# Kernel optimization log

Measured on AMD Instinct MI355X. Metric: run time of the kernel, lower is better.

The kernel has to match this reference:

```python
import jax, jax.numpy as jnp
import numpy as np

B, A, H = 128, 24, 256
N, E = B * A, B * A * A
MAX_ATOMS, TIME_DIM, TEXT_DIM, NFREQ, NLAYERS = 103, 256, 128, 10, 4
DIS_DIM = NFREQ * 2 * 3  # 60
EDGE_IN = 2 * H + 9 + DIS_DIM  # 581


def setup_inputs() -> dict:
    key = jax.random.key(0)
    ks = iter(jax.random.split(key, 40))
    def nrm(shape, fan_in):
        return jax.random.normal(next(ks), shape, jnp.float32) / np.sqrt(fan_in).astype(np.float32)
    # fully-connected block-diagonal edges per graph (incl. self-loops), as dense_to_sparse(block_diag(ones))
    ii = jnp.repeat(jnp.arange(A, dtype=jnp.int32), A)
    jj = jnp.tile(jnp.arange(A, dtype=jnp.int32), A)
    off = (jnp.arange(B, dtype=jnp.int32) * A)[:, None]
    edges = jnp.stack([(off + ii[None, :]).reshape(-1), (off + jj[None, :]).reshape(-1)])  # [2,E]
    node2graph = jnp.repeat(jnp.arange(B, dtype=jnp.int32), A)  # [N]
    edge2graph = node2graph[edges[0]]  # [E]
    return dict(
        atom_types=jax.random.normal(next(ks), (N, MAX_ATOMS), jnp.float32),
        frac_coords=jax.random.uniform(next(ks), (N, 3), jnp.float32),
        lattices=jax.random.normal(next(ks), (B, 3, 3), jnp.float32),
        t=jax.random.normal(next(ks), (B, TIME_DIM), jnp.float32),
        text_embeds=jax.random.normal(next(ks), (B, TEXT_DIM), jnp.float32),
        w_emb=nrm((H, MAX_ATOMS), MAX_ATOMS), b_emb=jnp.zeros((H,), jnp.float32),
        w_cond=nrm((2 * H, TIME_DIM + TEXT_DIM), TIME_DIM + TEXT_DIM), b_cond=jnp.zeros((2 * H,), jnp.float32),
        w_proj=nrm((H, H), H), b_proj=jnp.zeros((H,), jnp.float32),
        film_g=jnp.ones((H,), jnp.float32), film_b=jnp.zeros((H,), jnp.float32),
        edge_w1=nrm((NLAYERS, H, EDGE_IN), EDGE_IN), edge_b1=jnp.zeros((NLAYERS, H), jnp.float32),
        edge_w2=nrm((NLAYERS, H, H), H), edge_b2=jnp.zeros((NLAYERS, H), jnp.float32),
        node_w1=nrm((NLAYERS, H, 2 * H), 2 * H), node_b1=jnp.zeros((NLAYERS, H), jnp.float32),
        node_w2=nrm((NLAYERS, H, H), H), node_b2=jnp.zeros((NLAYERS, H), jnp.float32),
        w_coord=nrm((3, H), H), w_latt=nrm((9, H), H),
        w_type=nrm((MAX_ATOMS, H), H), b_type=jnp.zeros((MAX_ATOMS,), jnp.float32),
        edges=edges, node2graph=node2graph, edge2graph=edge2graph,
    )


def _layernorm(x, g, b):
    mu = jnp.mean(x, -1, keepdims=True)
    v = jnp.mean((x - mu) ** 2, -1, keepdims=True)
    return (x - mu) * jax.lax.rsqrt(v + 1e-5) * g + b


def reference(atom_types, frac_coords, lattices, t, text_embeds,
              w_emb, b_emb, w_cond, b_cond, w_proj, b_proj, film_g, film_b,
              edge_w1, edge_b1, edge_w2, edge_b2, node_w1, node_b1, node_w2, node_b2,
              w_coord, w_latt, w_type, b_type, edges, node2graph, edge2graph):
    silu = jax.nn.silu
    e0, e1 = edges[0], edges[1]
    # gen_edges (fc): periodic fractional difference per edge
    frac_diff = (frac_coords[e1] - frac_coords[e0]) % 1.0  # [E,3]
    # SinusoidsEmbedding (detached in the original)
    freqs = 2.0 * jnp.pi * jnp.arange(NFREQ, dtype=jnp.float32)
    emb = (frac_diff[..., None] * freqs).reshape(frac_diff.shape[0], 3 * NFREQ)
    demb = jax.lax.stop_gradient(jnp.concatenate([jnp.sin(emb), jnp.cos(emb)], -1))  # [E,60]
    # lattice inner products (ip=True), gathered per edge
    lat_ips = jnp.einsum('bij,bkj->bik', lattices, lattices).reshape(-1, 9)
    lat_e = lat_ips[edge2graph]  # [E,9]
    # FiLM conditioning (identical every layer) -- repeat_interleave per atom == gather by node2graph
    cond = silu(jnp.concatenate([t, text_embeds], -1) @ w_cond.T + b_cond)[node2graph]  # [N,2H]
    scale, shift = cond[:, :H], cond[:, H:]
    deg = jnp.maximum(jax.ops.segment_sum(jnp.ones((e0.shape[0],), jnp.float32), e0, num_segments=N), 1.0)
    nf = atom_types @ w_emb.T + b_emb  # smooth node embedding: Linear(max_atoms, H)
    for i in range(NLAYERS):
        # FiLM layer
        y = _layernorm(nf @ w_proj.T + b_proj, film_g, film_b)
        nf = nf + silu(y * scale + shift)
        # CSPLayer edge model: gather -> concat -> 2-layer MLP
        ein = jnp.concatenate([nf[e0], nf[e1], lat_e, demb], -1)  # [E, 581]
        ef = silu(ein @ edge_w1[i].T + edge_b1[i])
        ef = silu(ef @ edge_w2[i].T + edge_b2[i])
        # node model: scatter_mean over source nodes, then 2-layer MLP, residual
        agg = jax.ops.segment_sum(ef, e0, num_segments=N) / deg[:, None]
        no = silu(jnp.concatenate([nf, agg], -1) @ node_w1[i].T + node_b1[i])
        no = silu(no @ node_w2[i].T + node_b2[i])
        nf = nf + no
    coords_out = nf @ w_coord.T  # [N,3]
    gfeat = jax.ops.segment_sum(nf, node2graph, num_segments=B) / jnp.float32(A)  # scatter mean over graphs
    lattice_out = (gfeat @ w_latt.T).reshape(-1, 3, 3)
    lattice_out = jnp.einsum('bij,bjk->bik', lattice_out, lattices)  # ip=True
    atom_types_out = nf @ w_type.T + b_type  # [N,103]
    return atom_types_out, lattice_out, coords_out, nf
```

## Files before the change

### kernel.cpp

```cpp
#include <hip/hip_runtime.h>
#include <math.h>

#define B_      128
#define A_      24
#define N_      3072
#define NLAYERS 4

#define OFF_COND    0
#define OFF_LATW    65536
#define OFF_NFMIDH  196608
#define OFF_AGGH    589824
#define OFF_PARTIH  983040
#define OFF_PARTJH  1376256
#define OFF_W1LATT  1769472
#define OFF_PW1A    1778688
#define OFF_PW1B    1909760
#define OFF_PW1D    2040832
#define OFF_PW2     2073600
#define OFF_PWPROJ  2204672
#define OFF_PNW1    2237440
#define OFF_PNW2    2499584
#define OFF_PWEMB   2630656
#define OFF_PWCOND  2647040
#define OFF_PWTYPE  2745344

#define OUT_TYPES  0
#define OUT_LATT   316416
#define OUT_COORD  317568
#define OUT_NF     326784

typedef __attribute__((ext_vector_type(8))) short bf16x8;
typedef __attribute__((ext_vector_type(4))) float f32x4;

__device__ __forceinline__ float silu_f(float x) { return x / (1.0f + __expf(-x)); }
__device__ __forceinline__ unsigned short f2bf(float x) {
    unsigned int u = __float_as_uint(x);
    return (unsigned short)((u + 0x7FFFu + ((u >> 16) & 1u)) >> 16);
}
__device__ __forceinline__ float bf2f(unsigned short h) {
    return __uint_as_float(((unsigned int)h) << 16);
}

__global__ void k_prep(const float* w_emb, const float* w_cond, const float* w_proj,
                       const float* ew1, const float* ew2, const float* nw1, const float* nw2,
                       const float* w_type, float* ws) {
    int idx = blockIdx.x * blockDim.x + threadIdx.x;
    unsigned short* pu = (unsigned short*)ws;
    int i = idx;
    if (i < 9216)   { int l = i / 2304, r = (i % 2304) / 256, h = i % 256;
                      ws[OFF_W1LATT + i] = ew1[((size_t)l * 256 + h) * 581 + 512 + r]; return; }        i -= 9216;
    if (i < 262144) { int l = i >> 16, r = i & 65535, ks = r >> 13, r2 = r & 8191,
                      nt = r2 >> 9, r3 = r2 & 511, lane = r3 >> 3, j = r3 & 7;
                      int k = ks * 32 + (lane >> 4) * 8 + j, n = nt * 16 + (lane & 15);
                      pu[(size_t)OFF_PW1A * 2 + i] = f2bf(ew1[((size_t)l * 256 + n) * 581 + k]); return; } i -= 262144;
    if (i < 262144) { int l = i >> 16, r = i & 65535, ks = r >> 13, r2 = r & 8191,
                      nt = r2 >> 9, r3 = r2 & 511, lane = r3 >> 3, j = r3 & 7;
                      int k = ks * 32 + (lane >> 4) * 8 + j, n = nt * 16 + (lane & 15);
                      pu[(size_t)OFF_PW1B * 2 + i] = f2bf(ew1[((size_t)l * 256 + n) * 581 + 256 + k]); return; } i -= 262144;
    if (i < 65536)  { int l = i >> 14, r = i & 16383, ks = r >> 13, r2 = r & 8191,
                      nt = r2 >> 9, r3 = r2 & 511, lane = r3 >> 3, j = r3 & 7;
                      int kp = ks * 32 + (lane >> 4) * 8 + j, n = nt * 16 + (lane & 15);
                      float v = (kp < 60) ? ew1[((size_t)l * 256 + n) * 581 + 521 + kp] : 0.0f;
                      pu[(size_t)OFF_PW1D * 2 + i] = f2bf(v); return; }                                  i -= 65536;
    if (i < 262144) { int l = i >> 16, r = i & 65535, ks = r >> 13, r2 = r & 8191,
                      nt = r2 >> 9, r3 = r2 & 511, lane = r3 >> 3, j = r3 & 7;
                      int k = ks * 32 + (lane >> 4) * 8 + j, n = nt * 16 + (lane & 15);
                      pu[(size_t)OFF_PW2 * 2 + i] = f2bf(ew2[((size_t)l * 256 + n) * 256 + k]); return; } i -= 262144;
    if (i < 65536)  { int ks = i >> 13, r2 = i & 8191,
                      nt = r2 >> 9, r3 = r2 & 511, lane = r3 >> 3, j = r3 & 7;
                      int k = ks * 32 + (lane >> 4) * 8 + j, n = nt * 16 + (lane & 15);
                      pu[(size_t)OFF_PWPROJ * 2 + i] = f2bf(w_proj[(size_t)n * 256 + k]); return; }      i -= 65536;
    if (i < 524288) { int l = i >> 17, r = i & 131071, ks = r >> 13, r2 = r & 8191,
                      nt = r2 >> 9, r3 = r2 & 511, lane = r3 >> 3, j = r3 & 7;
                      int k = ks * 32 + (lane >> 4) * 8 + j, n = nt * 16 + (lane & 15);
                      pu[(size_t)OFF_PNW1 * 2 + i] = f2bf(nw1[((size_t)l * 256 + n) * 512 + k]); return; } i -= 524288;
    if (i < 262144) { int l = i >> 16, r = i & 65535, ks = r >> 13, r2 = r & 8191,
                      nt = r2 >> 9, r3 = r2 & 511, lane = r3 >> 3, j = r3 & 7;
                      int k = ks * 32 + (lane >> 4) * 8 + j, n = nt * 16 + (lane & 15);
                      pu[(size_t)OFF_PNW2 * 2 + i] = f2bf(nw2[((size_t)l * 256 + n) * 256 + k]); return; } i -= 262144;
    if (i < 32768)  { int ks = i >> 13, r2 = i & 8191,
                      nt = r2 >> 9, r3 = r2 & 511, lane = r3 >> 3, j = r3 & 7;
                      int k = ks * 32 + (lane >> 4) * 8 + j, n = nt * 16 + (lane & 15);
                      float v = (k < 103) ? w_emb[(size_t)n * 103 + k] : 0.0f;
                      pu[(size_t)OFF_PWEMB * 2 + i] = f2bf(v); return; }                                 i -= 32768;
    if (i < 196608) { int ks = i / 16384, r2 = i & 16383,
                      nt = r2 >> 9, r3 = r2 & 511, lane = r3 >> 3, j = r3 & 7;
                      int k = ks * 32 + (lane >> 4) * 8 + j, n = nt * 16 + (lane & 15);
                      pu[(size_t)OFF_PWCOND * 2 + i] = f2bf(w_cond[(size_t)n * 384 + k]); return; }      i -= 196608;
    { int ks = i / 3584, r2 = i % 3584,
      nt = r2 >> 9, r3 = r2 & 511, lane = r3 >> 3, j = r3 & 7;
      int k = ks * 32 + (lane >> 4) * 8 + j, a = nt * 16 + (lane & 15);
      float v = (a < 103) ? w_type[(size_t)a * 256 + k] : 0.0f;
      pu[(size_t)OFF_PWTYPE * 2 + i] = f2bf(v); }
}

__global__ void __launch_bounds__(256) k_setup(const float* lat, const float* t_in, const float* tx,
                                               const float* b_cond, float* ws) {
    __shared__ __align__(16) unsigned short s_ct[16][392];
    __shared__ float s_lat[16][9];
    int tid = threadIdx.x, w = tid >> 6, ln = tid & 63;
    int l15 = ln & 15, g = ln >> 4;
    int g0 = blockIdx.x * 16;
    if (tid < 144) {
        int gl = tid / 9, r = tid % 9, ii = r / 3, kk = r % 3;
        const float* L = lat + (g0 + gl) * 9;
        s_lat[gl][r] = L[ii*3+0]*L[kk*3+0] + L[ii*3+1]*L[kk*3+1] + L[ii*3+2]*L[kk*3+2];
    }
    for (int idx = tid; idx < 16 * 384; idx += 256) {
        int row = idx / 384, k = idx % 384;
        float v = (k < 256) ? t_in[(size_t)(g0 + row) * 256 + k] : tx[(size_t)(g0 + row) * 128 + (k - 256)];
        s_ct[row][k] = f2bf(v);
    }
    __syncthreads();
    for (int idx = tid; idx < 16384; idx += 256) {
        int l = idx >> 12, gl = (idx >> 8) & 15, h = idx & 255;
        float a = 0.f;
#pragma unroll
        for (int r = 0; r < 9; r++) a += s_lat[gl][r] * ws[OFF_W1LATT + (l * 9 + r) * 256 + h];
        ws[OFF_LATW + (size_t)(l * 128 + g0 + gl) * 256 + h] = a;
    }
    const unsigned short* pc = (const unsigned short*)ws + (size_t)OFF_PWCOND * 2;
    f32x4 acc[8] = {};
    for (int ks = 0; ks < 12; ks++) {
        bf16x8 a = *(const bf16x8*)&s_ct[l15][ks * 32 + g * 8];
#pragma unroll
        for (int q = 0; q < 8; q++) {
            int nt = w * 8 + q;
            bf16x8 bf = *(const bf16x8*)&pc[((size_t)(ks * 32 + nt) * 64 + ln) * 8];
            acc[q] = __builtin_amdgcn_mfma_f32_16x16x32_bf16(a, bf, acc[q], 0, 0, 0);
        }
    }
#pragma unroll
    for (int q = 0; q < 8; q++) {
        int col = w * 128 + q * 16 + l15;
        float bc = b_cond[col];
#pragma unroll
        for (int r = 0; r < 4; r++) {
            int gg = g0 + 4 * g + r;
            ws[OFF_COND + (size_t)gg * 512 + col] = silu_f(acc[q][r] + bc);
        }
    }
}

__global__ void __launch_bounds__(256) k_fnf(int l, const float* at, const float* b_emb,
                                             const float* nb1, const float* nb2,
                                             const float* b_proj, const float* film_g, const float* film_b,
                                             const float* eb1, float* ws) {
    __shared__ __align__(16) unsigned short s_in[16][536];
    __shared__ __align__(16) unsigned short s_h[16][264];
    __shared__ __align__(16) unsigned short s_a[16][264];
    __shared__ float s_nf[16][260];
    __shared__ float s_mu[16], s_rs[16];
    float (*s_c)[268] = (float(*)[268])&s_in[0][0];
    int tid = threadIdx.x, w = tid >> 6, ln = tid & 63;
    int l15 = ln & 15, g = ln >> 4;
    int n0 = blockIdx.x * 16;
    const unsigned short* wsu = (const unsigned short*)ws;
    unsigned short* wsw = (unsigned short*)ws;

    f32x4 accn[4] = {};
    if (l == 0) {
        for (int idx = tid; idx < 16 * 128; idx += 256) {
            int row = idx >> 7, k = idx & 127;
            s_in[row][k] = (k < 103) ? f2bf(at[(size_t)(n0 + row) * 103 + k]) : (unsigned short)0;
        }
        __syncthreads();
        const unsigned short* pe = wsu + (size_t)OFF_PWEMB * 2;
        for (int ks = 0; ks < 4; ks++) {
            bf16x8 a = *(const bf16x8*)&s_in[l15][ks * 32 + g * 8];
#pragma unroll
            for (int nt = 0; nt < 4; nt++) {
                bf16x8 bf = *(const bf16x8*)&pe[((size_t)(ks * 16 + w * 4 + nt) * 64 + ln) * 8];
                accn[nt] = __builtin_amdgcn_mfma_f32_16x16x32_bf16(a, bf, accn[nt], 0, 0, 0);
            }
        }
#pragma unroll
        for (int nt = 0; nt < 4; nt++) {
            int col = w * 64 + nt * 16 + l15;
            float be = b_emb[col];
#pragma unroll
            for (int r = 0; r < 4; r++) {
                int row = 4 * g + r;
                float v = accn[nt][r] + be;
                s_nf[row][col] = v;
                s_a[row][col] = f2bf(v);
            }
        }
    } else {
        int lp = l - 1;
        const unsigned short* nfmidh = wsu + (size_t)OFF_NFMIDH * 2;
        const unsigned short* aggh   = wsu + (size_t)OFF_AGGH * 2;
#pragma unroll
        for (int t = 0; t < 2; t++) {
            int idx = tid + t * 256;
            int row = idx >> 5, c8 = idx & 31;
            *(uint4*)&s_in[row][c8 * 8]       = *(const uint4*)&nfmidh[(size_t)(n0 + row) * 256 + c8 * 8];
            *(uint4*)&s_in[row][256 + c8 * 8] = *(const uint4*)&aggh[(size_t)(n0 + row) * 256 + c8 * 8];
        }
        __syncthreads();
        const unsigned short* p1 = wsu + (size_t)OFF_PNW1 * 2 + (size_t)lp * 131072;
        f32x4 acc[4] = {};
        for (int ks = 0; ks < 16; ks++) {
            bf16x8 a = *(const bf16x8*)&s_in[l15][ks * 32 + g * 8];
#pragma unroll
            for (int nt = 0; nt < 4; nt++) {
                bf16x8 bf = *(const bf16x8*)&p1[((size_t)(ks * 16 + w * 4 + nt) * 64 + ln) * 8];
                acc[nt] = __builtin_amdgcn_mfma_f32_16x16x32_bf16(a, bf, acc[nt], 0, 0, 0);
            }
        }
#pragma unroll
        for (int nt = 0; nt < 4; nt++) {
            int col = w * 64 + nt * 16 + l15;
            float b1 = nb1[lp * 256 + col];
#pragma unroll
            for (int r = 0; r < 4; r++) s_h[4 * g + r][col] = f2bf(silu_f(acc[nt][r] + b1));
        }
        __syncthreads();
        const unsigned short* p2 = wsu + (size_t)OFF_PNW2 * 2 + (size_t)lp * 65536;
        for (int ks = 0; ks < 8; ks++) {
            bf16x8 a = *(const bf16x8*)&s_h[l15][ks * 32 + g * 8];
#pragma unroll
            for (int nt = 0; nt < 4; nt++) {
                bf16x8 bf = *(const bf16x8*)&p2[((size_t)(ks * 16 + w * 4 + nt) * 64 + ln) * 8];
                accn[nt] = __builtin_amdgcn_mfma_f32_16x16x32_bf16(a, bf, accn[nt], 0, 0, 0);
            }
        }
#pragma unroll
        for (int nt = 0; nt < 4; nt++) {
            int col = w * 64 + nt * 16 + l15;
            float b2 = nb2[lp * 256 + col];
#pragma unroll
            for (int r = 0; r < 4; r++) {
                int row = 4 * g + r;
                float v = bf2f(s_in[row][col]) + silu_f(accn[nt][r] + b2);
                s_nf[row][col] = v;
                s_a[row][col] = f2bf(v);
            }
        }
    }
    __syncthreads();
    const unsigned short* pwp = wsu + (size_t)OFF_PWPROJ * 2;
    f32x4 accp[4] = {};
    for (int ks = 0; ks < 8; ks++) {
        bf16x8 a = *(const bf16x8*)&s_a[l15][ks * 32 + g * 8];
#pragma unroll
        for (int nt = 0; nt < 4; nt++) {
            bf16x8 bf = *(const bf16x8*)&pwp[((size_t)(ks * 16 + w * 4 + nt) * 64 + ln) * 8];
            accp[nt] = __builtin_amdgcn_mfma_f32_16x16x32_bf16(a, bf, accp[nt], 0, 0, 0);
        }
    }
#pragma unroll
    for (int nt = 0; nt < 4; nt++) {
        int col = w * 64 + nt * 16 + l15;
        float bp = b_proj[col];
#pragma unroll
        for (int r = 0; r < 4; r++) s_c[4 * g + r][col] = accp[nt][r] + bp;
    }
    __syncthreads();
    for (int r4 = 0; r4 < 4; r4++) {
        int row = w * 4 + r4;
        float s = 0.f, q = 0.f;
        for (int c = ln; c < 256; c += 64) { float v = s_c[row][c]; s += v; q += v * v; }
#pragma unroll
        for (int o = 1; o < 64; o <<= 1) { s += __shfl_xor(s, o); q += __shfl_xor(q, o); }
        if (ln == 0) {
            float mu = s * (1.0f / 256.0f);
            float var = q * (1.0f / 256.0f) - mu * mu;
            s_mu[row] = mu; s_rs[row] = rsqrtf(var + 1e-5f);
        }
    }
    __syncthreads();
    {
        float gg = film_g[tid], bb = film_b[tid];
        unsigned short* nfmidh = wsw + (size_t)OFF_NFMIDH * 2;
        for (int row = 0; row < 16; row++) {
            int n = n0 + row, b = n / 24;
            float sc = ws[OFF_COND + (size_t)b * 512 + tid];
            float sh = ws[OFF_COND + (size_t)b * 512 + 256 + tid];
            float yn = (s_c[row][tid] - s_mu[row]) * s_rs[row] * gg + bb;
            float outv = s_nf[row][tid] + silu_f(yn * sc + sh);
            unsigned short ob = f2bf(outv);
            nfmidh[(size_t)n * 256 + tid] = ob;
            s_a[row][tid] = ob;
        }
    }
    __syncthreads();
    const unsigned short* pA = wsu + (size_t)OFF_PW1A * 2 + (size_t)l * 65536;
    const unsigned short* pB = wsu + (size_t)OFF_PW1B * 2 + (size_t)l * 65536;
    f32x4 aI[4] = {}, aJ[4] = {};
    for (int ks = 0; ks < 8; ks++) {
        bf16x8 a = *(const bf16x8*)&s_a[l15][ks * 32 + g * 8];
#pragma unroll
        for (int nt = 0; nt < 4; nt++) {
            bf16x8 bi = *(const bf16x8*)&pA[((size_t)(ks * 16 + w * 4 + nt) * 64 + ln) * 8];
            bf16x8 bj = *(const bf16x8*)&pB[((size_t)(ks * 16 + w * 4 + nt) * 64 + ln) * 8];
            aI[nt] = __builtin_amdgcn_mfma_f32_16x16x32_bf16(a, bi, aI[nt], 0, 0, 0);
            aJ[nt] = __builtin_amdgcn_mfma_f32_16x16x32_bf16(a, bj, aJ[nt], 0, 0, 0);
        }
    }
    unsigned short* partih = wsw + (size_t)OFF_PARTIH * 2;
    unsigned short* partjh = wsw + (size_t)OFF_PARTJH * 2;
#pragma unroll
    for (int nt = 0; nt < 4; nt++) {
        int col = w * 64 + nt * 16 + l15;
        float e1 = eb1[l * 256 + col];
#pragma unroll
        for (int r = 0; r < 4; r++) {
            int n = n0 + 4 * g + r;
            int gb = n / 24;
            float vi = aI[nt][r] + e1 + ws[OFF_LATW + (size_t)(l * 128 + gb) * 256 + col];
            partih[(size_t)n * 256 + col] = f2bf(vi);
            partjh[(size_t)n * 256 + col] = f2bf(aJ[nt][r]);
        }
    }
}

__global__ void __launch_bounds__(256, 4) k_edge(int l, const float* frac, const float* eb2, float* ws) {
    __shared__ __align__(16) unsigned short s_u[48 * 256];
    __shared__ __align__(16) unsigned short s_pJ[24][264];
    __shared__ __align__(16) unsigned short s_pI[2][264];
    __shared__ float s_fc[24][3];
    int tid = threadIdx.x, w = tid >> 6, ln = tid & 63;
    int l15 = ln & 15, g = ln >> 4;
    int b = blockIdx.x & 127, c = blockIdx.x >> 7;
    int i0 = c * 2;

    const unsigned short* partjh = (const unsigned short*)ws + (size_t)OFF_PARTJH * 2 + (size_t)b * 24 * 256;
    const unsigned short* partih = (const unsigned short*)ws + (size_t)OFF_PARTIH * 2 + (size_t)(b * 24 + i0) * 256;
    for (int idx = tid; idx < 72; idx += 256) s_fc[idx / 3][idx % 3] = frac[b * 72 + idx];
    for (int idx = tid; idx < 768; idx += 256) {
        int row = idx >> 5, c8 = idx & 31;
        *(uint4*)&s_pJ[row][c8 * 8] = *(const uint4*)&partjh[row * 256 + c8 * 8];
    }
    if (tid < 64) {
        int row = tid >> 5, c8 = tid & 31;
        *(uint4*)&s_pI[row][c8 * 8] = *(const uint4*)&partih[row * 256 + c8 * 8];
    }
    __syncthreads();
    for (int idx = tid; idx < 3072; idx += 256) {
        int row = idx >> 6, k = idx & 63;
        unsigned short v = 0;
        if (k < 60) {
            int kk = (k < 30) ? k : k - 30;
            int d = kk / 10, f = kk % 10;
            int hi = (row >= 24);
            int j = row - (hi ? 24 : 0);
            float fd = s_fc[j][d] - s_fc[i0 + hi][d];
            fd -= floorf(fd);
            float ang = fd * (6.283185307179586f * (float)f);
            v = f2bf((k < 30) ? __sinf(ang) : __cosf(ang));
        }
        s_u[(row << 6) + (((k >> 3) ^ (row & 7)) << 3) + (k & 7)] = v;
    }
    __syncthreads();

    const unsigned short* wsu = (const unsigned short*)ws;
    const unsigned short* pw1d = wsu + (size_t)OFF_PW1D * 2 + (size_t)l * 16384;
    f32x4 acc[3][4] = {};
    for (int ks = 0; ks < 2; ks++) {
        bf16x8 a[3];
        int kb = ks * 4 + g;
#pragma unroll
        for (int mt = 0; mt < 3; mt++) {
            int row = mt * 16 + l15;
            a[mt] = *(const bf16x8*)&s_u[(row << 6) + ((kb ^ (row & 7)) << 3)];
        }
#pragma unroll
        for (int nt = 0; nt < 4; nt++) {
            bf16x8 bf = *(const bf16x8*)&pw1d[((size_t)(ks * 16 + w * 4 + nt) * 64 + ln) * 8];
#pragma unroll
            for (int mt = 0; mt < 3; mt++)
                acc[mt][nt] = __builtin_amdgcn_mfma_f32_16x16x32_bf16(a[mt], bf, acc[mt][nt], 0, 0, 0);
        }
    }
    __syncthreads();
    float pIv[2][4];
#pragma unroll
    for (int hi = 0; hi < 2; hi++)
#pragma unroll
        for (int nt = 0; nt < 4; nt++) pIv[hi][nt] = bf2f(s_pI[hi][w * 64 + nt * 16 + l15]);
#pragma unroll
    for (int mt = 0; mt < 3; mt++)
#pragma unroll
        for (int nt = 0; nt < 4; nt++) {
            int col = w * 64 + nt * 16 + l15;
#pragma unroll
            for (int r = 0; r < 4; r++) {
                int row = mt * 16 + 4 * g + r;
                int hi = (row >= 24);
                int j = row - 24 * hi;
                float v = acc[mt][nt][r] + pIv[hi][nt] + bf2f(s_pJ[j][col]);
                s_u[(row << 8) + ((((col >> 3) ^ (row & 7))) << 3) + (col & 7)] = f2bf(silu_f(v));
            }
        }
    __syncthreads();
    const unsigned short* pw2 = wsu + (size_t)OFF_PW2 * 2 + (size_t)l * 65536;
    f32x4 acc2[3][4] = {};
    for (int ks = 0; ks < 8; ks++) {
        bf16x8 a[3];
        int kb = ks * 4 + g;
#pragma unroll
        for (int mt = 0; mt < 3; mt++) {
            int row = mt * 16 + l15;
            a[mt] = *(const bf16x8*)&s_u[(row << 8) + ((kb ^ (row & 7)) << 3)];
        }
#pragma unroll
        for (int nt = 0; nt < 4; nt++) {
            bf16x8 bf = *(const bf16x8*)&pw2[((size_t)(ks * 16 + w * 4 + nt) * 64 + ln) * 8];
#pragma unroll
            for (int mt = 0; mt < 3; mt++)
                acc2[mt][nt] = __builtin_amdgcn_mfma_f32_16x16x32_bf16(a[mt], bf, acc2[mt][nt], 0, 0, 0);
        }
    }
    float s0[4] = {}, s1[4] = {};
#pragma unroll
    for (int nt = 0; nt < 4; nt++) {
        int col = w * 64 + nt * 16 + l15;
        float b2 = eb2[l * 256 + col];
#pragma unroll
        for (int r = 0; r < 4; r++) s0[nt] += silu_f(acc2[0][nt][r] + b2);
        float m = 0.f;
#pragma unroll
        for (int r = 0; r < 4; r++) m += silu_f(acc2[1][nt][r] + b2);
        if (g < 2) s0[nt] += m; else s1[nt] += m;
#pragma unroll
        for (int r = 0; r < 4; r++) s1[nt] += silu_f(acc2[2][nt][r] + b2);
    }
#pragma unroll
    for (int nt = 0; nt < 4; nt++) {
        s0[nt] += __shfl_xor(s0[nt], 16);
        s0[nt] += __shfl_xor(s0[nt], 32);
        s1[nt] += __shfl_xor(s1[nt], 16);
        s1[nt] += __shfl_xor(s1[nt], 32);
    }
    unsigned short* aggh = (unsigned short*)ws + (size_t)OFF_AGGH * 2;
    if (g == 0) {
#pragma unroll
        for (int nt = 0; nt < 4; nt++) {
            int col = w * 64 + nt * 16 + l15;
            aggh[(size_t)(b * 24 + i0) * 256 + col]     = f2bf(s0[nt] * (1.0f / 24.0f));
            aggh[(size_t)(b * 24 + i0 + 1) * 256 + col] = f2bf(s1[nt] * (1.0f / 24.0f));
        }
    }
}

__global__ void __launch_bounds__(256) k_tail(const float* nb1, const float* nb2,
                                              const float* b_type, const float* w_coord,
                                              float* ws, float* out) {
    __shared__ __align__(16) unsigned short s_in[16][536];
    __shared__ __align__(16) unsigned short s_h[16][264];
    __shared__ __align__(16) unsigned short s_a[16][264];
    __shared__ float s_nf[16][260];
    int tid = threadIdx.x, w = tid >> 6, ln = tid & 63;
    int l15 = ln & 15, g = ln >> 4;
    int n0 = blockIdx.x * 16;
    const unsigned short* wsu = (const unsigned short*)ws;
    const int lp = 3;
    const unsigned short* nfmidh = wsu + (size_t)OFF_NFMIDH * 2;
    const unsigned short* aggh   = wsu + (size_t)OFF_AGGH * 2;
#pragma unroll
    for (int t = 0; t < 2; t++) {
        int idx = tid + t * 256;
        int row = idx >> 5, c8 = idx & 31;
        *(uint4*)&s_in[row][c8 * 8]       = *(const uint4*)&nfmidh[(size_t)(n0 + row) * 256 + c8 * 8];
        *(uint4*)&s_in[row][256 + c8 * 8] = *(const uint4*)&aggh[(size_t)(n0 + row) * 256 + c8 * 8];
    }
    __syncthreads();
    const unsigned short* p1 = wsu + (size_t)OFF_PNW1 * 2 + (size_t)lp * 131072;
    f32x4 acc[4] = {};
    for (int ks = 0; ks < 16; ks++) {
        bf16x8 a = *(const bf16x8*)&s_in[l15][ks * 32 + g * 8];
#pragma unroll
        for (int nt = 0; nt < 4; nt++) {
            bf16x8 bf = *(const bf16x8*)&p1[((size_t)(ks * 16 + w * 4 + nt) * 64 + ln) * 8];
            acc[nt] = __builtin_amdgcn_mfma_f32_16x16x32_bf16(a, bf, acc[nt], 0, 0, 0);
        }
    }
#pragma unroll
    for (int nt = 0; nt < 4; nt++) {
        int col = w * 64 + nt * 16 + l15;
        float b1 = nb1[lp * 256 + col];
#pragma unroll
        for (int r = 0; r < 4; r++) s_h[4 * g + r][col] = f2bf(silu_f(acc[nt][r] + b1));
    }
    __syncthreads();
    const unsigned short* p2 = wsu + (size_t)OFF_PNW2 * 2 + (size_t)lp * 65536;
    f32x4 a2[4] = {};
    for (int ks = 0; ks < 8; ks++) {
        bf16x8 a = *(const bf16x8*)&s_h[l15][ks * 32 + g * 8];
#pragma unroll
        for (int nt = 0; nt < 4; nt++) {
            bf16x8 bf = *(const bf16x8*)&p2[((size_t)(ks * 16 + w * 4 + nt) * 64 + ln) * 8];
            a2[nt] = __builtin_amdgcn_mfma_f32_16x16x32_bf16(a, bf, a2[nt], 0, 0, 0);
        }
    }
#pragma unroll
    for (int nt = 0; nt < 4; nt++) {
        int col = w * 64 + nt * 16 + l15;
        float b2 = nb2[lp * 256 + col];
#pragma unroll
        for (int r = 0; r < 4; r++) {
            int row = 4 * g + r, n = n0 + row;
            float v = bf2f(s_in[row][col]) + silu_f(a2[nt][r] + b2);
            s_nf[row][col] = v;
            s_a[row][col] = f2bf(v);
            out[OUT_NF + (size_t)n * 256 + col] = v;
        }
    }
    __syncthreads();
    const unsigned short* pt = wsu + (size_t)OFF_PWTYPE * 2;
    f32x4 at2[2] = {};
    for (int ks = 0; ks < 8; ks++) {
        bf16x8 a = *(const bf16x8*)&s_a[l15][ks * 32 + g * 8];
#pragma unroll
        for (int q = 0; q < 2; q++) {
            int nt = w + 4 * q;
            if (nt < 7) {
                bf16x8 bf = *(const bf16x8*)&pt[((size_t)(ks * 7 + nt) * 64 + ln) * 8];
                at2[q] = __builtin_amdgcn_mfma_f32_16x16x32_bf16(a, bf, at2[q], 0, 0, 0);
            }
        }
    }
#pragma unroll
    for (int q = 0; q < 2; q++) {
        int nt = w + 4 * q;
        if (nt < 7) {
            int a_col = nt * 16 + l15;
            if (a_col < 103) {
                float bt = b_type[a_col];
#pragma unroll
                for (int r = 0; r < 4; r++) {
                    int n = n0 + 4 * g + r;
                    out[OUT_TYPES + (size_t)n * 103 + a_col] = at2[q][r] + bt;
                }
            }
        }
    }
    if (tid < 48) {
        int p = tid / 3, cc = tid % 3;
        float a0 = 0.f;
        for (int k = 0; k < 256; k++) a0 += s_nf[p][k] * w_coord[cc * 256 + k];
        out[OUT_COORD + (size_t)(n0 + p) * 3 + cc] = a0;
    }
}

__global__ void k_out_graph(const float* lattices, const float* w_latt, const float* out_nf, float* out) {
    __shared__ float gf[256];
    __shared__ float lo[9];
    int b = blockIdx.x, h = threadIdx.x;
    float g = 0.f;
#pragma unroll
    for (int i = 0; i < 24; i++) g += out_nf[OUT_NF + (size_t)(b * 24 + i) * 256 + h];
    gf[h] = g * (1.0f / 24.0f);
    __syncthreads();
    if (h < 9) {
        float a0 = 0.f;
        for (int k = 0; k < 256; k++) a0 += gf[k] * w_latt[h * 256 + k];
        lo[h] = a0;
    }
    __syncthreads();
    if (h < 9) {
        int i = h / 3, kk = h % 3;
        float a0 = 0.f;
#pragma unroll
        for (int j = 0; j < 3; j++) a0 += lo[i * 3 + j] * lattices[b * 9 + j * 3 + kk];
        out[OUT_LATT + b * 9 + h] = a0;
    }
}

extern "C" void kernel_launch(void* const* d_in, const int* in_sizes, int n_in,
                              void* d_out, int out_size, void* d_ws, size_t ws_size,
                              hipStream_t stream) {
    const float* atom_types = (const float*)d_in[0];
    const float* frac       = (const float*)d_in[1];
    const float* lattices   = (const float*)d_in[2];
    const float* t_in       = (const float*)d_in[3];
    const float* text       = (const float*)d_in[4];
    const float* w_emb      = (const float*)d_in[5];
    const float* b_emb      = (const float*)d_in[6];
    const float* w_cond     = (const float*)d_in[7];
    const float* b_cond     = (const float*)d_in[8];
    const float* w_proj     = (const float*)d_in[9];
    const float* b_proj     = (const float*)d_in[10];
    const float* film_g     = (const float*)d_in[11];
    const float* film_b     = (const float*)d_in[12];
    const float* ew1        = (const float*)d_in[13];
    const float* eb1        = (const float*)d_in[14];
    const float* ew2        = (const float*)d_in[15];
    const float* eb2        = (const float*)d_in[16];
    const float* nw1        = (const float*)d_in[17];
    const float* nb1        = (const float*)d_in[18];
    const float* nw2        = (const float*)d_in[19];
    const float* nb2        = (const float*)d_in[20];
    const float* w_coord    = (const float*)d_in[21];
    const float* w_latt     = (const float*)d_in[22];
    const float* w_type     = (const float*)d_in[23];
    const float* b_type     = (const float*)d_in[24];
    float* ws  = (float*)d_ws;
    float* out = (float*)d_out;

    k_prep<<<7700, 256, 0, stream>>>(w_emb, w_cond, w_proj, ew1, ew2, nw1, nw2, w_type, ws);
    k_setup<<<8, 256, 0, stream>>>(lattices, t_in, text, b_cond, ws);
    for (int l = 0; l < NLAYERS; l++) {
        k_fnf<<<N_ / 16, 256, 0, stream>>>(l, atom_types, b_emb, nb1, nb2,
                                           b_proj, film_g, film_b, eb1, ws);
        k_edge<<<N_ * 12 / 24, 256, 0, stream>>>(l, frac, eb2, ws);
    }
    k_tail<<<N_ / 16, 256, 0, stream>>>(nb1, nb2, b_type, w_coord, ws, out);
    k_out_graph<<<B_, 256, 0, stream>>>(lattices, w_latt, out, out);
}
```

Baseline: 376.0 us.

## Use 512-thread blocks in node kernels and fuse graph pooling into tail

The node-side kernel now runs with 8 wavefronts per block, each computing half as many output column tiles, which raises per-block parallelism and lowers per-thread accumulator registers. The tail kernel is regridded to one block per graph (24 rows padded to 32). It also absorbs the separate graph-mean and lattice-output kernel, removing one launch and the reread of node features from global memory. The cost is extra barriers, wasted MFMA work on the padded rows, and fewer blocks in the tail.

```diff
diff --git a/kernel.cpp b/kernel.cpp
--- a/kernel.cpp
+++ b/kernel.cpp
@@ -142,7 +142,7 @@
     }
 }
 
-__global__ void __launch_bounds__(256) k_fnf(int l, const float* at, const float* b_emb,
+__global__ void __launch_bounds__(512) k_fnf(int l, const float* at, const float* b_emb,
                                              const float* nb1, const float* nb2,
                                              const float* b_proj, const float* film_g, const float* film_b,
                                              const float* eb1, float* ws) {
@@ -158,9 +158,9 @@
     const unsigned short* wsu = (const unsigned short*)ws;
     unsigned short* wsw = (unsigned short*)ws;
 
-    f32x4 accn[4] = {};
+    f32x4 accn[2] = {};
     if (l == 0) {
-        for (int idx = tid; idx < 16 * 128; idx += 256) {
+        for (int idx = tid; idx < 16 * 128; idx += 512) {
             int row = idx >> 7, k = idx & 127;
             s_in[row][k] = (k < 103) ? f2bf(at[(size_t)(n0 + row) * 103 + k]) : (unsigned short)0;
         }
@@ -169,19 +169,20 @@
         for (int ks = 0; ks < 4; ks++) {
             bf16x8 a = *(const bf16x8*)&s_in[l15][ks * 32 + g * 8];
 #pragma unroll
-            for (int nt = 0; nt < 4; nt++) {
-                bf16x8 bf = *(const bf16x8*)&pe[((size_t)(ks * 16 + w * 4 + nt) * 64 + ln) * 8];
-                accn[nt] = __builtin_amdgcn_mfma_f32_16x16x32_bf16(a, bf, accn[nt], 0, 0, 0);
+            for (int q = 0; q < 2; q++) {
+                bf16x8 bf = *(const bf16x8*)&pe[((size_t)(ks * 16 + 2 * w + q) * 64 + ln) * 8];
+                accn[q] = __builtin_amdgcn_mfma_f32_16x16x32_bf16(a, bf, accn[q], 0, 0, 0);
             }
         }
-#pragma unroll
-        for (int nt = 0; nt < 4; nt++) {
-            int col = w * 64 + nt * 16 + l15;
+        __syncthreads();
+#pragma unroll
+        for (int q = 0; q < 2; q++) {
+            int col = w * 32 + q * 16 + l15;
             float be = b_emb[col];
 #pragma unroll
             for (int r = 0; r < 4; r++) {
                 int row = 4 * g + r;
-                float v = accn[nt][r] + be;
+                float v = accn[q][r] + be;
                 s_nf[row][col] = v;
                 s_a[row][col] = f2bf(v);
             }
@@ -190,49 +191,47 @@
         int lp = l - 1;
         const unsigned short* nfmidh = wsu + (size_t)OFF_NFMIDH * 2;
         const unsigned short* aggh   = wsu + (size_t)OFF_AGGH * 2;
-#pragma unroll
-        for (int t = 0; t < 2; t++) {
-            int idx = tid + t * 256;
-            int row = idx >> 5, c8 = idx & 31;
+        {
+            int row = tid >> 5, c8 = tid & 31;
             *(uint4*)&s_in[row][c8 * 8]       = *(const uint4*)&nfmidh[(size_t)(n0 + row) * 256 + c8 * 8];
             *(uint4*)&s_in[row][256 + c8 * 8] = *(const uint4*)&aggh[(size_t)(n0 + row) * 256 + c8 * 8];
         }
         __syncthreads();
         const unsigned short* p1 = wsu + (size_t)OFF_PNW1 * 2 + (size_t)lp * 131072;
-        f32x4 acc[4] = {};
+        f32x4 acc[2] = {};
         for (int ks = 0; ks < 16; ks++) {
             bf16x8 a = *(const bf16x8*)&s_in[l15][ks * 32 + g * 8];
 #pragma unroll
-            for (int nt = 0; nt < 4; nt++) {
-                bf16x8 bf = *(const bf16x8*)&p1[((size_t)(ks * 16 + w * 4 + nt) * 64 + ln) * 8];
-                acc[nt] = __builtin_amdgcn_mfma_f32_16x16x32_bf16(a, bf, acc[nt], 0, 0, 0);
+            for (int q = 0; q < 2; q++) {
+                bf16x8 bf = *(const bf16x8*)&p1[((size_t)(ks * 16 + 2 * w + q) * 64 + ln) * 8];
+                acc[q] = __builtin_amdgcn_mfma_f32_16x16x32_bf16(a, bf, acc[q], 0, 0, 0);
             }
         }
 #pragma unroll
-        for (int nt = 0; nt < 4; nt++) {
-            int col = w * 64 + nt * 16 + l15;
+        for (int q = 0; q < 2; q++) {
+            int col = w * 32 + q * 16 + l15;
             float b1 = nb1[lp * 256 + col];
 #pragma unroll
-            for (int r = 0; r < 4; r++) s_h[4 * g + r][col] = f2bf(silu_f(acc[nt][r] + b1));
+            for (int r = 0; r < 4; r++) s_h[4 * g + r][col] = f2bf(silu_f(acc[q][r] + b1));
         }
         __syncthreads();
         const unsigned short* p2 = wsu + (size_t)OFF_PNW2 * 2 + (size_t)lp * 65536;
         for (int ks = 0; ks < 8; ks++) {
             bf16x8 a = *(const bf16x8*)&s_h[l15][ks * 32 + g * 8];
 #pragma unroll
-            for (int nt = 0; nt < 4; nt++) {
-                bf16x8 bf = *(const bf16x8*)&p2[((size_t)(ks * 16 + w * 4 + nt) * 64 + ln) * 8];
-                accn[nt] = __builtin_amdgcn_mfma_f32_16x16x32_bf16(a, bf, accn[nt], 0, 0, 0);
+            for (int q = 0; q < 2; q++) {
+                bf16x8 bf = *(const bf16x8*)&p2[((size_t)(ks * 16 + 2 * w + q) * 64 + ln) * 8];
+                accn[q] = __builtin_amdgcn_mfma_f32_16x16x32_bf16(a, bf, accn[q], 0, 0, 0);
             }
         }
 #pragma unroll
-        for (int nt = 0; nt < 4; nt++) {
-            int col = w * 64 + nt * 16 + l15;
+        for (int q = 0; q < 2; q++) {
+            int col = w * 32 + q * 16 + l15;
             float b2 = nb2[lp * 256 + col];
 #pragma unroll
             for (int r = 0; r < 4; r++) {
                 int row = 4 * g + r;
-                float v = bf2f(s_in[row][col]) + silu_f(accn[nt][r] + b2);
+                float v = bf2f(s_in[row][col]) + silu_f(accn[q][r] + b2);
                 s_nf[row][col] = v;
                 s_a[row][col] = f2bf(v);
             }
@@ -240,25 +239,26 @@
     }
     __syncthreads();
     const unsigned short* pwp = wsu + (size_t)OFF_PWPROJ * 2;
-    f32x4 accp[4] = {};
+    f32x4 accp[2] = {};
     for (int ks = 0; ks < 8; ks++) {
         bf16x8 a = *(const bf16x8*)&s_a[l15][ks * 32 + g * 8];
 #pragma unroll
-        for (int nt = 0; nt < 4; nt++) {
-            bf16x8 bf = *(const bf16x8*)&pwp[((size_t)(ks * 16 + w * 4 + nt) * 64 + ln) * 8];
-            accp[nt] = __builtin_amdgcn_mfma_f32_16x16x32_bf16(a, bf, accp[nt], 0, 0, 0);
-        }
-    }
-#pragma unroll
-    for (int nt = 0; nt < 4; nt++) {
-        int col = w * 64 + nt * 16 + l15;
+        for (int q = 0; q < 2; q++) {
+            bf16x8 bf = *(const bf16x8*)&pwp[((size_t)(ks * 16 + 2 * w + q) * 64 + ln) * 8];
+            accp[q] = __builtin_amdgcn_mfma_f32_16x16x32_bf16(a, bf, accp[q], 0, 0, 0);
+        }
+    }
+    __syncthreads();
+#pragma unroll
+    for (int q = 0; q < 2; q++) {
+        int col = w * 32 + q * 16 + l15;
         float bp = b_proj[col];
 #pragma unroll
-        for (int r = 0; r < 4; r++) s_c[4 * g + r][col] = accp[nt][r] + bp;
-    }
-    __syncthreads();
-    for (int r4 = 0; r4 < 4; r4++) {
-        int row = w * 4 + r4;
+        for (int r = 0; r < 4; r++) s_c[4 * g + r][col] = accp[q][r] + bp;
+    }
+    __syncthreads();
+    for (int r2 = 0; r2 < 2; r2++) {
+        int row = w * 2 + r2;
         float s = 0.f, q = 0.f;
         for (int c = ln; c < 256; c += 64) { float v = s_c[row][c]; s += v; q += v * v; }
 #pragma unroll
@@ -271,46 +271,49 @@
     }
     __syncthreads();
     {
-        float gg = film_g[tid], bb = film_b[tid];
+        int col = tid & 255, rb = tid >> 8;
+        float gg = film_g[col], bb = film_b[col];
         unsigned short* nfmidh = wsw + (size_t)OFF_NFMIDH * 2;
-        for (int row = 0; row < 16; row++) {
+#pragma unroll
+        for (int t = 0; t < 8; t++) {
+            int row = rb + 2 * t;
             int n = n0 + row, b = n / 24;
-            float sc = ws[OFF_COND + (size_t)b * 512 + tid];
-            float sh = ws[OFF_COND + (size_t)b * 512 + 256 + tid];
-            float yn = (s_c[row][tid] - s_mu[row]) * s_rs[row] * gg + bb;
-            float outv = s_nf[row][tid] + silu_f(yn * sc + sh);
+            float sc = ws[OFF_COND + (size_t)b * 512 + col];
+            float sh = ws[OFF_COND + (size_t)b * 512 + 256 + col];
+            float yn = (s_c[row][col] - s_mu[row]) * s_rs[row] * gg + bb;
+            float outv = s_nf[row][col] + silu_f(yn * sc + sh);
             unsigned short ob = f2bf(outv);
-            nfmidh[(size_t)n * 256 + tid] = ob;
-            s_a[row][tid] = ob;
+            nfmidh[(size_t)n * 256 + col] = ob;
+            s_a[row][col] = ob;
         }
     }
     __syncthreads();
     const unsigned short* pA = wsu + (size_t)OFF_PW1A * 2 + (size_t)l * 65536;
     const unsigned short* pB = wsu + (size_t)OFF_PW1B * 2 + (size_t)l * 65536;
-    f32x4 aI[4] = {}, aJ[4] = {};
+    f32x4 aI[2] = {}, aJ[2] = {};
     for (int ks = 0; ks < 8; ks++) {
         bf16x8 a = *(const bf16x8*)&s_a[l15][ks * 32 + g * 8];
 #pragma unroll
-        for (int nt = 0; nt < 4; nt++) {
-            bf16x8 bi = *(const bf16x8*)&pA[((size_t)(ks * 16 + w * 4 + nt) * 64 + ln) * 8];
-            bf16x8 bj = *(const bf16x8*)&pB[((size_t)(ks * 16 + w * 4 + nt) * 64 + ln) * 8];
-            aI[nt] = __builtin_amdgcn_mfma_f32_16x16x32_bf16(a, bi, aI[nt], 0, 0, 0);
-            aJ[nt] = __builtin_amdgcn_mfma_f32_16x16x32_bf16(a, bj, aJ[nt], 0, 0, 0);
+        for (int q = 0; q < 2; q++) {
+            bf16x8 bi = *(const bf16x8*)&pA[((size_t)(ks * 16 + 2 * w + q) * 64 + ln) * 8];
+            bf16x8 bj = *(const bf16x8*)&pB[((size_t)(ks * 16 + 2 * w + q) * 64 + ln) * 8];
+            aI[q] = __builtin_amdgcn_mfma_f32_16x16x32_bf16(a, bi, aI[q], 0, 0, 0);
+            aJ[q] = __builtin_amdgcn_mfma_f32_16x16x32_bf16(a, bj, aJ[q], 0, 0, 0);
         }
     }
     unsigned short* partih = wsw + (size_t)OFF_PARTIH * 2;
     unsigned short* partjh = wsw + (size_t)OFF_PARTJH * 2;
 #pragma unroll
-    for (int nt = 0; nt < 4; nt++) {
-        int col = w * 64 + nt * 16 + l15;
+    for (int q = 0; q < 2; q++) {
+        int col = w * 32 + q * 16 + l15;
         float e1 = eb1[l * 256 + col];
 #pragma unroll
         for (int r = 0; r < 4; r++) {
             int n = n0 + 4 * g + r;
             int gb = n / 24;
-            float vi = aI[nt][r] + e1 + ws[OFF_LATW + (size_t)(l * 128 + gb) * 256 + col];
+            float vi = aI[q][r] + e1 + ws[OFF_LATW + (size_t)(l * 128 + gb) * 256 + col];
             partih[(size_t)n * 256 + col] = f2bf(vi);
-            partjh[(size_t)n * 256 + col] = f2bf(aJ[nt][r]);
+            partjh[(size_t)n * 256 + col] = f2bf(aJ[q][r]);
         }
     }
 }
@@ -444,127 +447,140 @@
     }
 }
 
-__global__ void __launch_bounds__(256) k_tail(const float* nb1, const float* nb2,
+__global__ void __launch_bounds__(512) k_tail(const float* nb1, const float* nb2,
                                               const float* b_type, const float* w_coord,
+                                              const float* lattices, const float* w_latt,
                                               float* ws, float* out) {
-    __shared__ __align__(16) unsigned short s_in[16][536];
-    __shared__ __align__(16) unsigned short s_h[16][264];
-    __shared__ __align__(16) unsigned short s_a[16][264];
-    __shared__ float s_nf[16][260];
+    __shared__ __align__(16) unsigned short s_in[32][536];
+    __shared__ __align__(16) unsigned short s_h[32][264];
+    __shared__ float gf[256];
+    __shared__ float lo[9];
+    float (*s_nf)[260] = (float(*)[260])&s_in[0][0];
+    unsigned short (*s_a)[264] = s_h;
     int tid = threadIdx.x, w = tid >> 6, ln = tid & 63;
     int l15 = ln & 15, g = ln >> 4;
-    int n0 = blockIdx.x * 16;
+    int b = blockIdx.x, n0 = b * 24;
     const unsigned short* wsu = (const unsigned short*)ws;
     const int lp = 3;
     const unsigned short* nfmidh = wsu + (size_t)OFF_NFMIDH * 2;
     const unsigned short* aggh   = wsu + (size_t)OFF_AGGH * 2;
-#pragma unroll
-    for (int t = 0; t < 2; t++) {
-        int idx = tid + t * 256;
+    for (int idx = tid; idx < 1024; idx += 512) {
         int row = idx >> 5, c8 = idx & 31;
-        *(uint4*)&s_in[row][c8 * 8]       = *(const uint4*)&nfmidh[(size_t)(n0 + row) * 256 + c8 * 8];
-        *(uint4*)&s_in[row][256 + c8 * 8] = *(const uint4*)&aggh[(size_t)(n0 + row) * 256 + c8 * 8];
+        int rr = (row < 24) ? row : 0;
+        *(uint4*)&s_in[row][c8 * 8]       = *(const uint4*)&nfmidh[(size_t)(n0 + rr) * 256 + c8 * 8];
+        *(uint4*)&s_in[row][256 + c8 * 8] = *(const uint4*)&aggh[(size_t)(n0 + rr) * 256 + c8 * 8];
     }
     __syncthreads();
     const unsigned short* p1 = wsu + (size_t)OFF_PNW1 * 2 + (size_t)lp * 131072;
-    f32x4 acc[4] = {};
+    f32x4 acc[2][2] = {};
     for (int ks = 0; ks < 16; ks++) {
-        bf16x8 a = *(const bf16x8*)&s_in[l15][ks * 32 + g * 8];
-#pragma unroll
-        for (int nt = 0; nt < 4; nt++) {
-            bf16x8 bf = *(const bf16x8*)&p1[((size_t)(ks * 16 + w * 4 + nt) * 64 + ln) * 8];
-            acc[nt] = __builtin_amdgcn_mfma_f32_16x16x32_bf16(a, bf, acc[nt], 0, 0, 0);
-        }
-    }
-#pragma unroll
-    for (int nt = 0; nt < 4; nt++) {
-        int col = w * 64 + nt * 16 + l15;
+        bf16x8 a0 = *(const bf16x8*)&s_in[l15][ks * 32 + g * 8];
+        bf16x8 a1 = *(const bf16x8*)&s_in[16 + l15][ks * 32 + g * 8];
+#pragma unroll
+        for (int q = 0; q < 2; q++) {
+            bf16x8 bf = *(const bf16x8*)&p1[((size_t)(ks * 16 + 2 * w + q) * 64 + ln) * 8];
+            acc[0][q] = __builtin_amdgcn_mfma_f32_16x16x32_bf16(a0, bf, acc[0][q], 0, 0, 0);
+            acc[1][q] = __builtin_amdgcn_mfma_f32_16x16x32_bf16(a1, bf, acc[1][q], 0, 0, 0);
+        }
+    }
+#pragma unroll
+    for (int q = 0; q < 2; q++) {
+        int col = w * 32 + q * 16 + l15;
         float b1 = nb1[lp * 256 + col];
 #pragma unroll
-        for (int r = 0; r < 4; r++) s_h[4 * g + r][col] = f2bf(silu_f(acc[nt][r] + b1));
+        for (int mt = 0; mt < 2; mt++)
+#pragma unroll
+            for (int r = 0; r < 4; r++) s_h[mt * 16 + 4 * g + r][col] = f2bf(silu_f(acc[mt][q][r] + b1));
     }
     __syncthreads();
     const unsigned short* p2 = wsu + (size_t)OFF_PNW2 * 2 + (size_t)lp * 65536;
-    f32x4 a2[4] = {};
+    f32x4 a2[2][2] = {};
     for (int ks = 0; ks < 8; ks++) {
-        bf16x8 a = *(const bf16x8*)&s_h[l15][ks * 32 + g * 8];
-#pragma unroll
-        for (int nt = 0; nt < 4; nt++) {
-            bf16x8 bf = *(const bf16x8*)&p2[((size_t)(ks * 16 + w * 4 + nt) * 64 + ln) * 8];
-            a2[nt] = __builtin_amdgcn_mfma_f32_16x16x32_bf16(a, bf, a2[nt], 0, 0, 0);
-        }
-    }
-#pragma unroll
-    for (int nt = 0; nt < 4; nt++) {
-        int col = w * 64 + nt * 16 + l15;
+        bf16x8 a0 = *(const bf16x8*)&s_h[l15][ks * 32 + g * 8];
+        bf16x8 a1 = *(const bf16x8*)&s_h[16 + l15][ks * 32 + g * 8];
+#pragma unroll
+        for (int q = 0; q < 2; q++) {
+            bf16x8 bf = *(const bf16x8*)&p2[((size_t)(ks * 16 + 2 * w + q) * 64 + ln) * 8];
+            a2[0][q] = __builtin_amdgcn_mfma_f32_16x16x32_bf16(a0, bf, a2[0][q], 0, 0, 0);
+            a2[1][q] = __builtin_amdgcn_mfma_f32_16x16x32_bf16(a1, bf, a2[1][q], 0, 0, 0);
+        }
+    }
+    float res[2][2][4];
+#pragma unroll
+    for (int q = 0; q < 2; q++) {
+        int col = w * 32 + q * 16 + l15;
+#pragma unroll
+        for (int mt = 0; mt < 2; mt++)
+#pragma unroll
+            for (int r = 0; r < 4; r++) res[mt][q][r] = bf2f(s_in[mt * 16 + 4 * g + r][col]);
+    }
+    __syncthreads();
+#pragma unroll
+    for (int q = 0; q < 2; q++) {
+        int col = w * 32 + q * 16 + l15;
         float b2 = nb2[lp * 256 + col];
 #pragma unroll
-        for (int r = 0; r < 4; r++) {
-            int row = 4 * g + r, n = n0 + row;
-            float v = bf2f(s_in[row][col]) + silu_f(a2[nt][r] + b2);
-            s_nf[row][col] = v;
-            s_a[row][col] = f2bf(v);
-            out[OUT_NF + (size_t)n * 256 + col] = v;
-        }
-    }
-    __syncthreads();
-    const unsigned short* pt = wsu + (size_t)OFF_PWTYPE * 2;
-    f32x4 at2[2] = {};
-    for (int ks = 0; ks < 8; ks++) {
-        bf16x8 a = *(const bf16x8*)&s_a[l15][ks * 32 + g * 8];
-#pragma unroll
-        for (int q = 0; q < 2; q++) {
-            int nt = w + 4 * q;
-            if (nt < 7) {
-                bf16x8 bf = *(const bf16x8*)&pt[((size_t)(ks * 7 + nt) * 64 + ln) * 8];
-                at2[q] = __builtin_amdgcn_mfma_f32_16x16x32_bf16(a, bf, at2[q], 0, 0, 0);
+        for (int mt = 0; mt < 2; mt++)
+#pragma unroll
+            for (int r = 0; r < 4; r++) {
+                int row = mt * 16 + 4 * g + r;
+                float v = res[mt][q][r] + silu_f(a2[mt][q][r] + b2);
+                if (row < 24) {
+                    s_nf[row][col] = v;
+                    out[OUT_NF + (size_t)(n0 + row) * 256 + col] = v;
+                }
+                s_a[row][col] = f2bf(v);
             }
-        }
-    }
-#pragma unroll
-    for (int q = 0; q < 2; q++) {
-        int nt = w + 4 * q;
-        if (nt < 7) {
-            int a_col = nt * 16 + l15;
-            if (a_col < 103) {
-                float bt = b_type[a_col];
+    }
+    __syncthreads();
+    if (w < 7) {
+        const unsigned short* pt = wsu + (size_t)OFF_PWTYPE * 2;
+        f32x4 at2[2] = {};
+        for (int ks = 0; ks < 8; ks++) {
+            bf16x8 a0 = *(const bf16x8*)&s_a[l15][ks * 32 + g * 8];
+            bf16x8 a1 = *(const bf16x8*)&s_a[16 + l15][ks * 32 + g * 8];
+            bf16x8 bf = *(const bf16x8*)&pt[((size_t)(ks * 7 + w) * 64 + ln) * 8];
+            at2[0] = __builtin_amdgcn_mfma_f32_16x16x32_bf16(a0, bf, at2[0], 0, 0, 0);
+            at2[1] = __builtin_amdgcn_mfma_f32_16x16x32_bf16(a1, bf, at2[1], 0, 0, 0);
+        }
+        int a_col = w * 16 + l15;
+        if (a_col < 103) {
+            float bt = b_type[a_col];
+#pragma unroll
+            for (int mt = 0; mt < 2; mt++)
 #pragma unroll
                 for (int r = 0; r < 4; r++) {
-                    int n = n0 + 4 * g + r;
-                    out[OUT_TYPES + (size_t)n * 103 + a_col] = at2[q][r] + bt;
+                    int row = mt * 16 + 4 * g + r;
+                    if (row < 24)
+                        out[OUT_TYPES + (size_t)(n0 + row) * 103 + a_col] = at2[mt][r] + bt;
                 }
-            }
-        }
-    }
-    if (tid < 48) {
+        }
+    }
+    if (tid < 72) {
         int p = tid / 3, cc = tid % 3;
         float a0 = 0.f;
         for (int k = 0; k < 256; k++) a0 += s_nf[p][k] * w_coord[cc * 256 + k];
         out[OUT_COORD + (size_t)(n0 + p) * 3 + cc] = a0;
     }
-}
-
-__global__ void k_out_graph(const float* lattices, const float* w_latt, const float* out_nf, float* out) {
-    __shared__ float gf[256];
-    __shared__ float lo[9];
-    int b = blockIdx.x, h = threadIdx.x;
-    float g = 0.f;
-#pragma unroll
-    for (int i = 0; i < 24; i++) g += out_nf[OUT_NF + (size_t)(b * 24 + i) * 256 + h];
-    gf[h] = g * (1.0f / 24.0f);
-    __syncthreads();
-    if (h < 9) {
+    if (tid < 256) {
+        float s = 0.f;
+#pragma unroll
+        for (int i = 0; i < 24; i++) s += s_nf[i][tid];
+        gf[tid] = s * (1.0f / 24.0f);
+    }
+    __syncthreads();
+    if (tid < 9) {
         float a0 = 0.f;
-        for (int k = 0; k < 256; k++) a0 += gf[k] * w_latt[h * 256 + k];
-        lo[h] = a0;
-    }
-    __syncthreads();
-    if (h < 9) {
-        int i = h / 3, kk = h % 3;
+        for (int k = 0; k < 256; k++) a0 += gf[k] * w_latt[tid * 256 + k];
+        lo[tid] = a0;
+    }
+    __syncthreads();
+    if (tid < 9) {
+        int i = tid / 3, kk = tid % 3;
         float a0 = 0.f;
 #pragma unroll
         for (int j = 0; j < 3; j++) a0 += lo[i * 3 + j] * lattices[b * 9 + j * 3 + kk];
-        out[OUT_LATT + b * 9 + h] = a0;
+        out[OUT_LATT + (size_t)b * 9 + tid] = a0;
     }
 }
 
@@ -602,10 +618,9 @@
     k_prep<<<7700, 256, 0, stream>>>(w_emb, w_cond, w_proj, ew1, ew2, nw1, nw2, w_type, ws);
     k_setup<<<8, 256, 0, stream>>>(lattices, t_in, text, b_cond, ws);
     for (int l = 0; l < NLAYERS; l++) {
-        k_fnf<<<N_ / 16, 256, 0, stream>>>(l, atom_types, b_emb, nb1, nb2,
+        k_fnf<<<N_ / 16, 512, 0, stream>>>(l, atom_types, b_emb, nb1, nb2,
                                            b_proj, film_g, film_b, eb1, ws);
         k_edge<<<N_ * 12 / 24, 256, 0, stream>>>(l, frac, eb2, ws);
     }
-    k_tail<<<N_ / 16, 256, 0, stream>>>(nb1, nb2, b_type, w_coord, ws, out);
-    k_out_graph<<<B_, 256, 0, stream>>>(lattices, w_latt, out, out);
-}
+    k_tail<<<B_, 512, 0, stream>>>(nb1, nb2, b_type, w_coord, lattices, w_latt, ws, out);
+}
```

After: 348.8 us. -7.2%, faster.
